# Kernel optimization log

Measured on AMD Instinct MI355X. Metric: run time of the kernel, lower is better.

The kernel has to match this reference:

```python
import jax, jax.numpy as jnp
import numpy as np

B, N, ENC, DEC, ATT = 32, 4096, 1024, 512, 512


def setup_inputs() -> dict:
    key = jax.random.key(0)
    ks = jax.random.split(key, 8)
    s_enc = 1.0 / np.sqrt(ENC)
    s_dec = 1.0 / np.sqrt(DEC)
    s_att = 1.0 / np.sqrt(ATT)
    return {
        "encoder_out": jax.random.normal(ks[0], (B, N, ENC), jnp.float32),
        "decoder_hidden": jax.random.normal(ks[1], (B, DEC), jnp.float32),
        "W_enc": jax.random.uniform(ks[2], (ENC, ATT), jnp.float32, -s_enc, s_enc),
        "b_enc": jax.random.uniform(ks[3], (ATT,), jnp.float32, -s_enc, s_enc),
        "W_dec": jax.random.uniform(ks[4], (DEC, ATT), jnp.float32, -s_dec, s_dec),
        "b_dec": jax.random.uniform(ks[5], (ATT,), jnp.float32, -s_dec, s_dec),
        "w_full": jax.random.uniform(ks[6], (ATT,), jnp.float32, -s_att, s_att),
        "b_full": jax.random.uniform(ks[7], (), jnp.float32, -s_att, s_att),
    }


def reference(encoder_out, decoder_hidden, W_enc, b_enc, W_dec, b_dec, w_full, b_full):
    # att1: [B, N, ATT]; att2: [B, 1, ATT]
    att1 = jnp.einsum('bne,ea->bna', encoder_out, W_enc) + b_enc
    att2 = (decoder_hidden @ W_dec + b_dec)[:, None, :]
    att = jax.nn.relu(att1 + att2)
    e = jnp.einsum('bna,a->bn', att, w_full) + b_full  # [B, N]
    alpha = jax.nn.softmax(e, axis=1)
    awe = jnp.einsum('bne,bn->be', encoder_out, alpha)  # weighted encoding [B, ENC]
    return awe, alpha
```

## Files before the change

kernel.cpp:

```cpp
#include <hip/hip_runtime.h>

#define B_ 32
#define N_ 4096
#define ENC_ 1024
#define DEC_ 512
#define ATT_ 512

typedef __attribute__((ext_vector_type(8))) short short8;
typedef __attribute__((ext_vector_type(4))) short short4v;
typedef __attribute__((ext_vector_type(4))) float f32x4;

__device__ __forceinline__ short f2bf(float f) {
  union { float f; unsigned u; } x; x.f = f;
  unsigned r = (x.u + 0x7FFFu + ((x.u >> 16) & 1u)) >> 16;
  return (short)r;
}

__device__ __forceinline__ void lds_barrier() {
  asm volatile("s_waitcnt lgkmcnt(0)" ::: "memory");
  __builtin_amdgcn_s_barrier();
  asm volatile("" ::: "memory");
}

extern "C" __global__ void __launch_bounds__(256) prep_kernel(
    const float* __restrict__ dh, const float* __restrict__ W_dec,
    const float* __restrict__ b_dec, const float* __restrict__ b_enc,
    const float* __restrict__ W_enc,
    float* __restrict__ att2, short* __restrict__ Wfrag)
{
  if (blockIdx.x < B_) {
    __shared__ float dhs[DEC_];
    int b = blockIdx.x;
    for (int i = threadIdx.x; i < DEC_; i += 256) dhs[i] = dh[b * DEC_ + i];
    __syncthreads();
    for (int a = threadIdx.x; a < ATT_; a += 256) {
      float s = b_dec[a] + b_enc[a];
      for (int k = 0; k < DEC_; ++k) s += dhs[k] * W_dec[k * ATT_ + a];
      att2[b * ATT_ + a] = s;
    }
  } else {
    int idx = (blockIdx.x - B_) * 256 + threadIdx.x;
    int l = idx & 63;
    int t = (idx >> 6) & 31;
    int c = idx >> 11;
    int col = c * 16 + (l & 15);
    int kb = t * 32 + (l >> 4) * 8;
    short8 p;
#pragma unroll
    for (int j = 0; j < 8; ++j) p[j] = f2bf(W_enc[(kb + j) * ATT_ + col]);
    *(short8*)(Wfrag + ((long)idx << 3)) = p;
  }
}

extern "C" __global__ void __launch_bounds__(512, 4) gemm_e_kernel(
    const float* __restrict__ enc, const short* __restrict__ Wfrag,
    const float* __restrict__ att2, const float* __restrict__ w_full,
    float* __restrict__ e_out)
{
  __shared__ __align__(16) short As[2][64 * 32];
  __shared__ float e_red[64][8];

  const int tid = threadIdx.x;
  const int lane = tid & 63;
  const int w = tid >> 6;
  const int blk = blockIdx.x;
  const int b = blk >> 6;
  const int n0 = (blk & 63) * 64;

  const int arow = tid >> 3;
  const int akc = tid & 7;
  const float* aptr = enc + ((long)(b * N_ + n0 + arow)) * ENC_ + akc * 4;
  const int awbyte = (arow * 64 + akc * 8) ^ ((arow & 7) << 4);

  int arbyte[4];
#pragma unroll
  for (int r = 0; r < 4; ++r) {
    int rr = r * 16 + (lane & 15);
    arbyte[r] = (rr * 64 + ((lane >> 4) * 16)) ^ ((rr & 7) << 4);
  }

  const short* bptr = Wfrag + (long)(w * 4) * 16384 + lane * 8;

  f32x4 acc[4][4] = {};
  short8 bfg[4];
  f32x4 pA0, pA1;

  {
    f32x4 a0 = *(const f32x4*)(aptr);
    short4v q;
#pragma unroll
    for (int j = 0; j < 4; ++j) q[j] = f2bf(a0[j]);
    *(short4v*)((char*)(&As[0][0]) + awbyte) = q;
  }
  pA0 = *(const f32x4*)(aptr + 32);
  pA1 = *(const f32x4*)(aptr + 64);
#pragma unroll
  for (int cc = 0; cc < 4; ++cc)
    bfg[cc] = *(const short8*)(bptr + cc * 16384);
  lds_barrier();

#define GBODY(CUR, NXT, T)                                                  \
  {                                                                         \
    short8 af[4];                                                           \
    _Pragma("unroll")                                                       \
    for (int r = 0; r < 4; ++r)                                             \
      af[r] = *(const short8*)((const char*)(&As[CUR][0]) + arbyte[r]);     \
    __builtin_amdgcn_s_setprio(1);                                          \
    _Pragma("unroll")                                                       \
    for (int cc = 0; cc < 4; ++cc) {                                        \
      _Pragma("unroll")                                                     \
      for (int r = 0; r < 4; ++r)                                           \
        acc[r][cc] = __builtin_amdgcn_mfma_f32_16x16x32_bf16(               \
            af[r], bfg[cc], acc[r][cc], 0, 0, 0);                           \
    }                                                                       \
    __builtin_amdgcn_s_setprio(0);                                          \
    if ((T) < 31) {                                                         \
      short4v qq;                                                           \
      _Pragma("unroll")                                                     \
      for (int j = 0; j < 4; ++j) qq[j] = f2bf(pA0[j]);                     \
      *(short4v*)((char*)(&As[NXT][0]) + awbyte) = qq;                      \
      pA0 = pA1;                                                            \
      _Pragma("unroll")                                                     \
      for (int cc = 0; cc < 4; ++cc)                                        \
        bfg[cc] = *(const short8*)(bptr + cc * 16384 + ((T) + 1) * 512);    \
    }                                                                       \
    if ((T) < 29) pA1 = *(const f32x4*)(aptr + ((T) + 3) * 32);             \
    if ((T) < 31) lds_barrier();                                            \
  }

  for (int tt = 0; tt < 32; tt += 2) {
    GBODY(0, 1, tt);
    GBODY(1, 0, tt + 1);
  }
#undef GBODY

  const int lq = lane >> 4, lr = lane & 15;
  float at2v[4], wv[4];
#pragma unroll
  for (int c = 0; c < 4; ++c) {
    int col = w * 64 + c * 16 + lr;
    at2v[c] = att2[b * ATT_ + col];
    wv[c] = w_full[col];
  }
#pragma unroll
  for (int r = 0; r < 4; ++r) {
#pragma unroll
    for (int j = 0; j < 4; ++j) {
      float s = 0.f;
#pragma unroll
      for (int c = 0; c < 4; ++c)
        s += fmaxf(acc[r][c][j] + at2v[c], 0.f) * wv[c];
      s += __shfl_xor(s, 1); s += __shfl_xor(s, 2);
      s += __shfl_xor(s, 4); s += __shfl_xor(s, 8);
      if (lr == 0) e_red[r * 16 + lq * 4 + j][w] = s;
    }
  }
  __syncthreads();
  if (tid < 64) {
    float ev = 0.f;
#pragma unroll
    for (int ww = 0; ww < 8; ++ww) ev += e_red[tid][ww];
    e_out[b * N_ + n0 + tid] = ev;
  }
}

extern "C" __global__ void __launch_bounds__(256) softmax_kernel(
    const float* __restrict__ e, float* __restrict__ alpha)
{
  int b = blockIdx.x, tid = threadIdx.x;
  float v[16];
  float m = -1e30f;
#pragma unroll
  for (int i = 0; i < 16; ++i) {
    v[i] = e[b * N_ + i * 256 + tid];
    m = fmaxf(m, v[i]);
  }
  for (int off = 1; off < 64; off <<= 1) m = fmaxf(m, __shfl_xor(m, off));
  __shared__ float redm[4];
  if ((tid & 63) == 0) redm[tid >> 6] = m;
  __syncthreads();
  m = fmaxf(fmaxf(redm[0], redm[1]), fmaxf(redm[2], redm[3]));
  float s = 0.f;
#pragma unroll
  for (int i = 0; i < 16; ++i) { v[i] = expf(v[i] - m); s += v[i]; }
  for (int off = 1; off < 64; off <<= 1) s += __shfl_xor(s, off);
  __shared__ float reds[4];
  if ((tid & 63) == 0) reds[tid >> 6] = s;
  __syncthreads();
  s = reds[0] + reds[1] + reds[2] + reds[3];
  float inv = 1.0f / s;
#pragma unroll
  for (int i = 0; i < 16; ++i) alpha[b * N_ + i * 256 + tid] = v[i] * inv;
}

extern "C" __global__ void __launch_bounds__(256) awe_part_kernel(
    const float* __restrict__ enc, const float* __restrict__ alpha,
    float* __restrict__ part)
{
  __shared__ float als[256];
  __shared__ f32x4 red[256];
  int bi = blockIdx.x;
  int b = bi & 31, cchunk = (bi >> 5) & 3, nchunk = bi >> 7;
  int t = threadIdx.x;
  int n0 = nchunk * 256;
  als[t] = alpha[b * N_ + n0 + t];
  __syncthreads();
  int tcol = t & 63, tn = t >> 6;
  const float* base = enc + (long)b * N_ * ENC_ + (long)n0 * ENC_ +
                      cchunk * 256 + tcol * 4;
  f32x4 acc = {};
  for (int i = tn; i < 256; i += 4) {
    f32x4 vv = *(const f32x4*)(base + (long)i * ENC_);
    acc += als[i] * vv;
  }
  red[t] = acc;
  __syncthreads();
  if (t < 64) {
    f32x4 s = red[t] + red[t + 64] + red[t + 128] + red[t + 192];
    *(f32x4*)(&part[(long)nchunk * 32768 + b * 1024 + cchunk * 256 + t * 4]) = s;
  }
}

extern "C" __global__ void __launch_bounds__(256) awe_reduce_kernel(
    const float* __restrict__ part, float* __restrict__ awe)
{
  int i = blockIdx.x * 256 + threadIdx.x;
  float s = 0.f;
#pragma unroll
  for (int p = 0; p < 16; ++p) s += part[(long)p * 32768 + i];
  awe[i] = s;
}

extern "C" void kernel_launch(void* const* d_in, const int* in_sizes, int n_in,
                              void* d_out, int out_size, void* d_ws, size_t ws_size,
                              hipStream_t stream) {
  const float* enc    = (const float*)d_in[0];
  const float* dh     = (const float*)d_in[1];
  const float* W_enc  = (const float*)d_in[2];
  const float* b_enc  = (const float*)d_in[3];
  const float* W_dec  = (const float*)d_in[4];
  const float* b_dec  = (const float*)d_in[5];
  const float* w_full = (const float*)d_in[6];
  float* out = (float*)d_out;

  char* ws = (char*)d_ws;
  float* att2  = (float*)ws;
  short* Wfrag = (short*)(ws + 65536);
  float* e_buf = (float*)(ws + 65536 + 1048576);
  float* part  = (float*)(ws + 65536 + 1048576 + 524288);

  hipLaunchKernelGGL(prep_kernel, dim3(B_ + 256), dim3(256), 0, stream,
                     dh, W_dec, b_dec, b_enc, W_enc, att2, Wfrag);
  hipLaunchKernelGGL(gemm_e_kernel, dim3(2048), dim3(512), 0, stream,
                     enc, Wfrag, att2, w_full, e_buf);
  hipLaunchKernelGGL(softmax_kernel, dim3(B_), dim3(256), 0, stream,
                     e_buf, out + B_ * ENC_);
  hipLaunchKernelGGL(awe_part_kernel, dim3(2048), dim3(256), 0, stream,
                     enc, out + B_ * ENC_, part);
  hipLaunchKernelGGL(awe_reduce_kernel, dim3(128), dim3(256), 0, stream,
                     part, out);
}
```

Baseline: 320.9 us.

## Load encoder A-fragments directly from global into registers, dropping LDS staging

Drops the shared-memory staging of the encoder tile and the per-step barriers. Each wave now loads its own fp32 A fragments straight from global memory, converts them to bf16 in registers and double-buffers both the A and B fragments in registers. This removes LDS traffic and synchronisation, but all 8 waves in a block now load the same A rows redundantly (8x more global/L2 reads), and register pressure rises. The occupancy hint in launch_bounds is also dropped.

```diff
diff --git a/kernel.cpp b/kernel.cpp
--- a/kernel.cpp
+++ b/kernel.cpp
@@ -7,19 +7,12 @@
 #define ATT_ 512
 
 typedef __attribute__((ext_vector_type(8))) short short8;
-typedef __attribute__((ext_vector_type(4))) short short4v;
 typedef __attribute__((ext_vector_type(4))) float f32x4;
 
 __device__ __forceinline__ short f2bf(float f) {
   union { float f; unsigned u; } x; x.f = f;
   unsigned r = (x.u + 0x7FFFu + ((x.u >> 16) & 1u)) >> 16;
   return (short)r;
-}
-
-__device__ __forceinline__ void lds_barrier() {
-  asm volatile("s_waitcnt lgkmcnt(0)" ::: "memory");
-  __builtin_amdgcn_s_barrier();
-  asm volatile("" ::: "memory");
 }
 
 extern "C" __global__ void __launch_bounds__(256) prep_kernel(
@@ -52,12 +45,11 @@
   }
 }
 
-extern "C" __global__ void __launch_bounds__(512, 4) gemm_e_kernel(
+extern "C" __global__ void __launch_bounds__(512) gemm_e_kernel(
     const float* __restrict__ enc, const short* __restrict__ Wfrag,
     const float* __restrict__ att2, const float* __restrict__ w_full,
     float* __restrict__ e_out)
 {
-  __shared__ __align__(16) short As[2][64 * 32];
   __shared__ float e_red[64][8];
 
   const int tid = threadIdx.x;
@@ -67,65 +59,56 @@
   const int b = blk >> 6;
   const int n0 = (blk & 63) * 64;
 
-  const int arow = tid >> 3;
-  const int akc = tid & 7;
-  const float* aptr = enc + ((long)(b * N_ + n0 + arow)) * ENC_ + akc * 4;
-  const int awbyte = (arow * 64 + akc * 8) ^ ((arow & 7) << 4);
-
-  int arbyte[4];
+  const float* afp[4];
+#pragma unroll
+  for (int r = 0; r < 4; ++r)
+    afp[r] = enc + (long)(b * N_ + n0 + r * 16 + (lane & 15)) * ENC_ +
+             ((lane >> 4) * 8);
+
+  const short* bptr = Wfrag + (long)(w * 4) * 16384 + lane * 8;
+
+  f32x4 acc[4][4] = {};
+  f32x4 pA[2][8];
+  short8 bfg[2][4];
+
 #pragma unroll
   for (int r = 0; r < 4; ++r) {
-    int rr = r * 16 + (lane & 15);
-    arbyte[r] = (rr * 64 + ((lane >> 4) * 16)) ^ ((rr & 7) << 4);
-  }
-
-  const short* bptr = Wfrag + (long)(w * 4) * 16384 + lane * 8;
-
-  f32x4 acc[4][4] = {};
-  short8 bfg[4];
-  f32x4 pA0, pA1;
-
-  {
-    f32x4 a0 = *(const f32x4*)(aptr);
-    short4v q;
-#pragma unroll
-    for (int j = 0; j < 4; ++j) q[j] = f2bf(a0[j]);
-    *(short4v*)((char*)(&As[0][0]) + awbyte) = q;
-  }
-  pA0 = *(const f32x4*)(aptr + 32);
-  pA1 = *(const f32x4*)(aptr + 64);
+    pA[0][2 * r] = *(const f32x4*)(afp[r]);
+    pA[0][2 * r + 1] = *(const f32x4*)(afp[r] + 4);
+  }
 #pragma unroll
   for (int cc = 0; cc < 4; ++cc)
-    bfg[cc] = *(const short8*)(bptr + cc * 16384);
-  lds_barrier();
-
-#define GBODY(CUR, NXT, T)                                                  \
-  {                                                                         \
-    short8 af[4];                                                           \
-    _Pragma("unroll")                                                       \
-    for (int r = 0; r < 4; ++r)                                             \
-      af[r] = *(const short8*)((const char*)(&As[CUR][0]) + arbyte[r]);     \
-    __builtin_amdgcn_s_setprio(1);                                          \
-    _Pragma("unroll")                                                       \
-    for (int cc = 0; cc < 4; ++cc) {                                        \
-      _Pragma("unroll")                                                     \
-      for (int r = 0; r < 4; ++r)                                           \
-        acc[r][cc] = __builtin_amdgcn_mfma_f32_16x16x32_bf16(               \
-            af[r], bfg[cc], acc[r][cc], 0, 0, 0);                           \
-    }                                                                       \
-    __builtin_amdgcn_s_setprio(0);                                          \
-    if ((T) < 31) {                                                         \
-      short4v qq;                                                           \
-      _Pragma("unroll")                                                     \
-      for (int j = 0; j < 4; ++j) qq[j] = f2bf(pA0[j]);                     \
-      *(short4v*)((char*)(&As[NXT][0]) + awbyte) = qq;                      \
-      pA0 = pA1;                                                            \
-      _Pragma("unroll")                                                     \
-      for (int cc = 0; cc < 4; ++cc)                                        \
-        bfg[cc] = *(const short8*)(bptr + cc * 16384 + ((T) + 1) * 512);    \
-    }                                                                       \
-    if ((T) < 29) pA1 = *(const f32x4*)(aptr + ((T) + 3) * 32);             \
-    if ((T) < 31) lds_barrier();                                            \
+    bfg[0][cc] = *(const short8*)(bptr + cc * 16384);
+
+#define GBODY(CUR, NXT, T)                                                    \
+  {                                                                           \
+    if ((T) + 1 < 32) {                                                       \
+      _Pragma("unroll")                                                       \
+      for (int r = 0; r < 4; ++r) {                                           \
+        pA[NXT][2 * r] = *(const f32x4*)(afp[r] + ((T) + 1) * 32);            \
+        pA[NXT][2 * r + 1] = *(const f32x4*)(afp[r] + ((T) + 1) * 32 + 4);    \
+      }                                                                       \
+      _Pragma("unroll")                                                       \
+      for (int cc = 0; cc < 4; ++cc)                                          \
+        bfg[NXT][cc] =                                                        \
+            *(const short8*)(bptr + cc * 16384 + ((T) + 1) * 512);            \
+    }                                                                         \
+    short8 afb[4];                                                            \
+    _Pragma("unroll")                                                         \
+    for (int r = 0; r < 4; ++r) {                                             \
+      _Pragma("unroll")                                                       \
+      for (int j = 0; j < 4; ++j) {                                           \
+        afb[r][j] = f2bf(pA[CUR][2 * r][j]);                                  \
+        afb[r][j + 4] = f2bf(pA[CUR][2 * r + 1][j]);                          \
+      }                                                                       \
+    }                                                                         \
+    _Pragma("unroll")                                                         \
+    for (int cc = 0; cc < 4; ++cc) {                                          \
+      _Pragma("unroll")                                                       \
+      for (int r = 0; r < 4; ++r)                                             \
+        acc[r][cc] = __builtin_amdgcn_mfma_f32_16x16x32_bf16(                 \
+            afb[r], bfg[CUR][cc], acc[r][cc], 0, 0, 0);                       \
+    }                                                                         \
   }
 
   for (int tt = 0; tt < 32; tt += 2) {
```

Result: slower. 749.6 us (+133.6%).

## Restructure encoder GEMM into persistent blocks staging half-K row slabs in LDS

Applied to the files above, without the earlier changes.

The GEMM kernel now launches 256 persistent blocks, each walking 8 consecutive 64-row tiles. For each tile it stages half of the K dimension (512 columns) in padded LDS buffers through large batched global loads, double-buffered across the two halves, so there are far fewer barriers than the old per-32-K step scheme. Fp32-to-bf16 conversion now uses the packed v_cvt_pk_bf16_f32 instruction, and the B fragments are double-buffered in registers. In exchange, LDS use and register pressure rise sharply (occupancy bound dropped to 2), and the grid is much smaller.

```diff
diff --git a/kernel.cpp b/kernel.cpp
--- a/kernel.cpp
+++ b/kernel.cpp
@@ -5,17 +5,22 @@
 #define ENC_ 1024
 #define DEC_ 512
 #define ATT_ 512
+#define ROWSTR 1040
 
 typedef __attribute__((ext_vector_type(8))) short short8;
-typedef __attribute__((ext_vector_type(4))) short short4v;
 typedef __attribute__((ext_vector_type(4))) float f32x4;
+typedef __attribute__((ext_vector_type(4))) unsigned u32x4;
 
 __device__ __forceinline__ short f2bf(float f) {
   union { float f; unsigned u; } x; x.f = f;
   unsigned r = (x.u + 0x7FFFu + ((x.u >> 16) & 1u)) >> 16;
   return (short)r;
 }
-
+__device__ __forceinline__ unsigned cvtpk(float a, float b) {
+  unsigned r;
+  asm("v_cvt_pk_bf16_f32 %0, %1, %2" : "=v"(r) : "v"(a), "v"(b));
+  return r;
+}
 __device__ __forceinline__ void lds_barrier() {
   asm volatile("s_waitcnt lgkmcnt(0)" ::: "memory");
   __builtin_amdgcn_s_barrier();
@@ -41,10 +46,10 @@
   } else {
     int idx = (blockIdx.x - B_) * 256 + threadIdx.x;
     int l = idx & 63;
-    int t = (idx >> 6) & 31;
+    int g = (idx >> 6) & 31;
     int c = idx >> 11;
     int col = c * 16 + (l & 15);
-    int kb = t * 32 + (l >> 4) * 8;
+    int kb = g * 32 + (l >> 4) * 8;
     short8 p;
 #pragma unroll
     for (int j = 0; j < 8; ++j) p[j] = f2bf(W_enc[(kb + j) * ATT_ + col]);
@@ -52,87 +57,31 @@
   }
 }
 
-extern "C" __global__ void __launch_bounds__(512, 4) gemm_e_kernel(
+extern "C" __global__ void __launch_bounds__(512, 2) gemm_e_kernel(
     const float* __restrict__ enc, const short* __restrict__ Wfrag,
     const float* __restrict__ att2, const float* __restrict__ w_full,
     float* __restrict__ e_out)
 {
-  __shared__ __align__(16) short As[2][64 * 32];
+  __shared__ __align__(16) short As[2][64 * (ROWSTR / 2)];
   __shared__ float e_red[64][8];
 
   const int tid = threadIdx.x;
   const int lane = tid & 63;
   const int w = tid >> 6;
   const int blk = blockIdx.x;
-  const int b = blk >> 6;
-  const int n0 = (blk & 63) * 64;
-
-  const int arow = tid >> 3;
-  const int akc = tid & 7;
-  const float* aptr = enc + ((long)(b * N_ + n0 + arow)) * ENC_ + akc * 4;
-  const int awbyte = (arow * 64 + akc * 8) ^ ((arow & 7) << 4);
-
-  int arbyte[4];
-#pragma unroll
-  for (int r = 0; r < 4; ++r) {
-    int rr = r * 16 + (lane & 15);
-    arbyte[r] = (rr * 64 + ((lane >> 4) * 16)) ^ ((rr & 7) << 4);
-  }
+  const int b = blk >> 3;
+
+  const int srow = tid >> 3;
+  const int sseg = tid & 7;
+  const int awb = srow * ROWSTR + sseg * 128;
+  const float* apRun = enc + ((long)(blk * 512 + srow)) * ENC_ + sseg * 64;
+
+  int arb[4];
+#pragma unroll
+  for (int r = 0; r < 4; ++r)
+    arb[r] = (r * 16 + (lane & 15)) * ROWSTR + (lane >> 4) * 16;
 
   const short* bptr = Wfrag + (long)(w * 4) * 16384 + lane * 8;
-
-  f32x4 acc[4][4] = {};
-  short8 bfg[4];
-  f32x4 pA0, pA1;
-
-  {
-    f32x4 a0 = *(const f32x4*)(aptr);
-    short4v q;
-#pragma unroll
-    for (int j = 0; j < 4; ++j) q[j] = f2bf(a0[j]);
-    *(short4v*)((char*)(&As[0][0]) + awbyte) = q;
-  }
-  pA0 = *(const f32x4*)(aptr + 32);
-  pA1 = *(const f32x4*)(aptr + 64);
-#pragma unroll
-  for (int cc = 0; cc < 4; ++cc)
-    bfg[cc] = *(const short8*)(bptr + cc * 16384);
-  lds_barrier();
-
-#define GBODY(CUR, NXT, T)                                                  \
-  {                                                                         \
-    short8 af[4];                                                           \
-    _Pragma("unroll")                                                       \
-    for (int r = 0; r < 4; ++r)                                             \
-      af[r] = *(const short8*)((const char*)(&As[CUR][0]) + arbyte[r]);     \
-    __builtin_amdgcn_s_setprio(1);                                          \
-    _Pragma("unroll")                                                       \
-    for (int cc = 0; cc < 4; ++cc) {                                        \
-      _Pragma("unroll")                                                     \
-      for (int r = 0; r < 4; ++r)                                           \
-        acc[r][cc] = __builtin_amdgcn_mfma_f32_16x16x32_bf16(               \
-            af[r], bfg[cc], acc[r][cc], 0, 0, 0);                           \
-    }                                                                       \
-    __builtin_amdgcn_s_setprio(0);                                          \
-    if ((T) < 31) {                                                         \
-      short4v qq;                                                           \
-      _Pragma("unroll")                                                     \
-      for (int j = 0; j < 4; ++j) qq[j] = f2bf(pA0[j]);                     \
-      *(short4v*)((char*)(&As[NXT][0]) + awbyte) = qq;                      \
-      pA0 = pA1;                                                            \
-      _Pragma("unroll")                                                     \
-      for (int cc = 0; cc < 4; ++cc)                                        \
-        bfg[cc] = *(const short8*)(bptr + cc * 16384 + ((T) + 1) * 512);    \
-    }                                                                       \
-    if ((T) < 29) pA1 = *(const f32x4*)(aptr + ((T) + 3) * 32);             \
-    if ((T) < 31) lds_barrier();                                            \
-  }
-
-  for (int tt = 0; tt < 32; tt += 2) {
-    GBODY(0, 1, tt);
-    GBODY(1, 0, tt + 1);
-  }
-#undef GBODY
 
   const int lq = lane >> 4, lr = lane & 15;
   float at2v[4], wv[4];
@@ -142,26 +91,104 @@
     at2v[c] = att2[b * ATT_ + col];
     wv[c] = w_full[col];
   }
-#pragma unroll
-  for (int r = 0; r < 4; ++r) {
-#pragma unroll
-    for (int j = 0; j < 4; ++j) {
-      float s = 0.f;
-#pragma unroll
-      for (int c = 0; c < 4; ++c)
-        s += fmaxf(acc[r][c][j] + at2v[c], 0.f) * wv[c];
-      s += __shfl_xor(s, 1); s += __shfl_xor(s, 2);
-      s += __shfl_xor(s, 4); s += __shfl_xor(s, 8);
-      if (lr == 0) e_red[r * 16 + lq * 4 + j][w] = s;
+
+  f32x4 pA[16];
+
+#define ISSUE_A(PTR)                                                          \
+  {                                                                           \
+    _Pragma("unroll")                                                         \
+    for (int j = 0; j < 16; ++j) pA[j] = *(const f32x4*)((PTR) + j * 4);      \
+  }
+
+#define CVT_WRITE(BUF)                                                        \
+  {                                                                           \
+    _Pragma("unroll")                                                         \
+    for (int u = 0; u < 8; ++u) {                                             \
+      union { u32x4 uu; short8 ss; } q;                                       \
+      q.uu[0] = cvtpk(pA[2 * u][0], pA[2 * u][1]);                            \
+      q.uu[1] = cvtpk(pA[2 * u][2], pA[2 * u][3]);                            \
+      q.uu[2] = cvtpk(pA[2 * u + 1][0], pA[2 * u + 1][1]);                    \
+      q.uu[3] = cvtpk(pA[2 * u + 1][2], pA[2 * u + 1][3]);                    \
+      *(short8*)((char*)&As[BUF][0] + awb + u * 16) = q.ss;                   \
+    }                                                                         \
+  }
+
+#define COMPUTE(BUF, G0, DO_ISSUE, APTR)                                      \
+  {                                                                           \
+    short8 Bb[2][4];                                                          \
+    _Pragma("unroll")                                                         \
+    for (int cc = 0; cc < 4; ++cc)                                            \
+      Bb[0][cc] = *(const short8*)(bptr + cc * 16384 + (G0) * 512);           \
+    _Pragma("unroll")                                                         \
+    for (int c = 0; c < 16; ++c) {                                            \
+      const int cb = c & 1, nb = cb ^ 1;                                      \
+      if (c < 15) {                                                           \
+        _Pragma("unroll")                                                     \
+        for (int cc = 0; cc < 4; ++cc)                                        \
+          Bb[nb][cc] =                                                        \
+              *(const short8*)(bptr + cc * 16384 + ((G0) + c + 1) * 512);     \
+      }                                                                       \
+      __builtin_amdgcn_sched_barrier(0);                                      \
+      if (c == 8 && (DO_ISSUE)) { ISSUE_A(APTR); }                            \
+      __builtin_amdgcn_sched_barrier(0);                                      \
+      short8 af[4];                                                           \
+      _Pragma("unroll")                                                       \
+      for (int r = 0; r < 4; ++r)                                             \
+        af[r] = *(const short8*)((const char*)&As[BUF][0] + arb[r] + c * 64); \
+      __builtin_amdgcn_s_setprio(1);                                          \
+      _Pragma("unroll")                                                       \
+      for (int cc = 0; cc < 4; ++cc) {                                        \
+        _Pragma("unroll")                                                     \
+        for (int r = 0; r < 4; ++r)                                           \
+          acc[r][cc] = __builtin_amdgcn_mfma_f32_16x16x32_bf16(               \
+              af[r], Bb[cb][cc], acc[r][cc], 0, 0, 0);                        \
+      }                                                                       \
+      __builtin_amdgcn_s_setprio(0);                                          \
+    }                                                                         \
+  }
+
+  ISSUE_A(apRun);
+  CVT_WRITE(0);
+  lds_barrier();
+
+#pragma unroll 1
+  for (int i = 0; i < 8; ++i) {
+    f32x4 acc[4][4] = {};
+
+    COMPUTE(0, 0, 1, apRun + 512);
+    CVT_WRITE(1);
+    lds_barrier();
+
+    const int more = (i < 7);
+    COMPUTE(1, 16, more, apRun + 65536);
+    if (more) CVT_WRITE(0);
+
+#pragma unroll
+    for (int r = 0; r < 4; ++r) {
+#pragma unroll
+      for (int j = 0; j < 4; ++j) {
+        float s = 0.f;
+#pragma unroll
+        for (int c = 0; c < 4; ++c)
+          s += fmaxf(acc[r][c][j] + at2v[c], 0.f) * wv[c];
+        s += __shfl_xor(s, 1); s += __shfl_xor(s, 2);
+        s += __shfl_xor(s, 4); s += __shfl_xor(s, 8);
+        if (lr == 0) e_red[r * 16 + lq * 4 + j][w] = s;
+      }
     }
-  }
-  __syncthreads();
-  if (tid < 64) {
-    float ev = 0.f;
-#pragma unroll
-    for (int ww = 0; ww < 8; ++ww) ev += e_red[tid][ww];
-    e_out[b * N_ + n0 + tid] = ev;
-  }
+    __syncthreads();
+    if (tid < 64) {
+      float ev = 0.f;
+#pragma unroll
+      for (int ww = 0; ww < 8; ++ww) ev += e_red[tid][ww];
+      int ti = blk * 8 + i;
+      e_out[b * N_ + (ti & 63) * 64 + tid] = ev;
+    }
+    apRun += 65536;
+  }
+#undef COMPUTE
+#undef CVT_WRITE
+#undef ISSUE_A
 }
 
 extern "C" __global__ void __launch_bounds__(256) softmax_kernel(
@@ -251,7 +278,7 @@
 
   hipLaunchKernelGGL(prep_kernel, dim3(B_ + 256), dim3(256), 0, stream,
                      dh, W_dec, b_dec, b_enc, W_enc, att2, Wfrag);
-  hipLaunchKernelGGL(gemm_e_kernel, dim3(2048), dim3(512), 0, stream,
+  hipLaunchKernelGGL(gemm_e_kernel, dim3(256), dim3(512), 0, stream,
                      enc, Wfrag, att2, w_full, e_buf);
   hipLaunchKernelGGL(softmax_kernel, dim3(B_), dim3(256), 0, stream,
                      e_buf, out + B_ * ENC_);
```

Result: slower. 761.0 us (+137.1%).
